# Kernel tuning notes

Hardware: AMD Instinct MI355X
Metric: run time of the kernel (lower is better)

Reference implementation:

```python
import jax, jax.numpy as jnp
import numpy as np

N, L, E, H = 8, 2048, 1024, 1024
EPS = 1e-5


def layernorm(x, g, b):
    m = jnp.mean(x, axis=-1, keepdims=True)
    v = jnp.var(x, axis=-1, keepdims=True)
    return (x - m) * jax.lax.rsqrt(v + EPS) * g + b


def setup_inputs() -> dict:
    key = jax.random.key(0)
    ks = jax.random.split(key, 6)
    s = 0.02
    return {
        "X": jax.random.normal(ks[0], (N, L, E), dtype=jnp.float32),
        "Wq": jax.random.normal(ks[1], (E, H), dtype=jnp.float32) * s,
        "bq": jnp.zeros((H,), jnp.float32),
        "Wk": jax.random.normal(ks[2], (E, H), dtype=jnp.float32) * s,
        "bk": jnp.zeros((H,), jnp.float32),
        "Wv": jax.random.normal(ks[3], (E, H), dtype=jnp.float32) * s,
        "bv": jnp.zeros((H,), jnp.float32),
        "Wf": jax.random.normal(ks[4], (H, H), dtype=jnp.float32) * s,
        "bf": jnp.zeros((H,), jnp.float32),
        "g1": jnp.ones((H,), jnp.float32),
        "b1": jnp.zeros((H,), jnp.float32),
        "g2": jnp.ones((H,), jnp.float32),
        "b2": jnp.zeros((H,), jnp.float32),
    }


def reference(X, Wq, bq, Wk, bk, Wv, bv, Wf, bf, g1, b1, g2, b2):
    scale = 1.0 / jnp.sqrt(jnp.float32(H))
    # both Q and K scaled by 1/sqrt(H) as in source (effective 1/H)
    Q = (X @ Wq + bq) * scale          # (N, L, H)
    K = (X @ Wk + bk) * scale          # (N, L, H)
    V = X @ Wv + bv                    # (N, L, H)
    A = jnp.einsum('nah,nbh->nab', Q, K)   # (N, Lq, Lk)
    A = jax.nn.softmax(A, axis=1)           # softmax over QUERY axis (dim=1), as in source
    # einsum('nll,nlh->nlh') = diagonal of A scaling V elementwise
    diag = jnp.diagonal(A, axis1=1, axis2=2)  # (N, L)
    O = diag[..., None] * V                   # (N, L, H)
    h = layernorm(O + X, g1, b1)
    h = layernorm(h @ Wf + bf + h, g2, b2)
    return h
```

## Files before the change

kernel.cpp:

```cpp
#include <hip/hip_runtime.h>
#include <math.h>

#define NB   8
#define LLEN 2048
#define HDIM 1024
#define LNEPS 1e-5f

#define BM 128
#define BK 64
#define NT_K (HDIM / BK)
#define NT_K8 (HDIM / 128)
#define NTHR 256
#define TB 16384

typedef __attribute__((ext_vector_type(8))) short short8;
typedef __attribute__((ext_vector_type(4))) unsigned short ushort4v;
typedef __attribute__((ext_vector_type(4))) float f32x4;
typedef __attribute__((ext_vector_type(4))) int int4v;
typedef __attribute__((ext_vector_type(8))) int int8v;
typedef __attribute__((ext_vector_type(8))) unsigned char uchar8;

typedef __attribute__((address_space(3))) void lds_void;
typedef const __attribute__((address_space(1))) void glob_void;

__device__ __forceinline__ unsigned short f2bf(float f) {
    union { float f; unsigned u; } v; v.f = f;
    unsigned r = v.u + 0x7FFFu + ((v.u >> 16) & 1u);
    return (unsigned short)(r >> 16);
}
__device__ __forceinline__ float bf2f(unsigned short h) {
    union { unsigned u; float f; } v; v.u = ((unsigned)h) << 16;
    return v.f;
}

__device__ __forceinline__ unsigned char f2fp8(float x) {
    union { float f; unsigned u; } v; v.f = x;
    unsigned s = (v.u >> 24) & 0x80u;
    float a = fabsf(x);
    if (!(a < 448.f)) return (unsigned char)(s | 0x7E);
    int e = (int)((v.u >> 23) & 0xFF) - 127;
    if (e < -6) e = -6;
    float q = rintf(ldexpf(a, 3 - e));
    if (q >= 16.f) { q *= 0.5f; e += 1; }
    int qi = (int)q;
    unsigned byte = (qi < 8) ? (unsigned)qi
                             : (((unsigned)(e + 7) << 3) | (unsigned)(qi - 8));
    return (unsigned char)(s | byte);
}
__device__ __forceinline__ float fp8d(unsigned char b) {
    int e = (b >> 3) & 15, m = b & 7;
    float v = e ? ldexpf((float)(8 + m), e - 10) : ldexpf((float)m, -9);
    return (b & 0x80) ? -v : v;
}

__device__ __forceinline__ unsigned pack4_fp8(float a, float b, float c, float d) {
#if __has_builtin(__builtin_amdgcn_cvt_pk_fp8_f32)
    int r = __builtin_amdgcn_cvt_pk_fp8_f32(a, b, 0, false);
    r = __builtin_amdgcn_cvt_pk_fp8_f32(c, d, r, true);
    return (unsigned)r;
#else
    return (unsigned)f2fp8(a) | ((unsigned)f2fp8(b) << 8)
         | ((unsigned)f2fp8(c) << 16) | ((unsigned)f2fp8(d) << 24);
#endif
}

__device__ __forceinline__ void wg_barrier() {
    asm volatile("" ::: "memory");
    __builtin_amdgcn_s_barrier();
    asm volatile("" ::: "memory");
}

__device__ __forceinline__ void stage128_bf16(
    const unsigned short* __restrict__ src, int R0, int kcol0,
    unsigned short* ldsDst, int w, int l)
{
    const int rsub = l >> 3;
    const int ce = 8 * ((l & 7) ^ rsub);
    #pragma unroll
    for (int s = 0; s < 4; ++s) {
        const int r = s*32 + w*8 + rsub;
        __builtin_amdgcn_global_load_lds(
            (glob_void*)(src + (size_t)(R0 + r) * HDIM + kcol0 + ce),
            (lds_void*)(ldsDst + s*2048 + w*512), 16, 0, 0);
    }
}

__device__ __forceinline__ void stage128_fp8(
    const unsigned char* __restrict__ src, int R0, int kcol0,
    unsigned char* ldsDst, int w, int l)
{
    const int rsub = l >> 3;
    const int cb = ((l & 7) ^ rsub) << 4;
    #pragma unroll
    for (int s = 0; s < 4; ++s) {
        const int r = s*32 + w*8 + rsub;
        __builtin_amdgcn_global_load_lds(
            (glob_void*)(src + (size_t)(R0 + r) * HDIM + kcol0 + cb),
            (lds_void*)(ldsDst + s*4096 + w*1024), 16, 0, 0);
    }
}

__device__ __forceinline__ void pipe128_bf16(
    const unsigned short* __restrict__ srcA,
    const unsigned short* __restrict__ srcB,
    int rowBase, int colBase, int k0, int nt,
    unsigned short* lds, f32x4 (&acc)[4][4])
{
    const int t = threadIdx.x, w = t >> 6, l = t & 63;
    const int wr = w >> 1, wc = w & 1;
    const int lr = l & 15;
    const int sw = (l & 7) << 4;
    const int aRB = (wr*64 + lr) * 128;
    const int bRB = (wc*64 + lr) * 128;
    const int c0 = ((l >> 4) * 16) ^ sw;
    const int c1 = (64 + ((l >> 4) * 16)) ^ sw;

    unsigned short* sA[2] = { lds,          lds + 2*(TB/2) };
    unsigned short* sB[2] = { lds + TB/2,   lds + 3*(TB/2) };

    stage128_bf16(srcA, rowBase, k0,      sA[0], w, l);
    stage128_bf16(srcB, colBase, k0,      sB[0], w, l);
    stage128_bf16(srcA, rowBase, k0 + BK, sA[1], w, l);
    stage128_bf16(srcB, colBase, k0 + BK, sB[1], w, l);
    asm volatile("s_waitcnt vmcnt(8)" ::: "memory");
    wg_barrier();

    for (int kt = 0; kt < nt; ++kt) {
        const char* bufA = (const char*)sA[kt & 1];
        const char* bufB = (const char*)sB[kt & 1];
        #pragma unroll
        for (int kk = 0; kk < 2; ++kk) {
            const int cc = kk ? c1 : c0;
            short8 af[4], bfr[4];
            #pragma unroll
            for (int mi = 0; mi < 4; ++mi)
                af[mi] = *(const short8*)(bufA + aRB + mi*2048 + cc);
            #pragma unroll
            for (int ni = 0; ni < 4; ++ni)
                bfr[ni] = *(const short8*)(bufB + bRB + ni*2048 + cc);
            #pragma unroll
            for (int mi = 0; mi < 4; ++mi)
                #pragma unroll
                for (int ni = 0; ni < 4; ++ni)
                    acc[mi][ni] = __builtin_amdgcn_mfma_f32_16x16x32_bf16(
                        af[mi], bfr[ni], acc[mi][ni], 0, 0, 0);
        }
        if (kt == nt - 1) break;
        wg_barrier();
        if (kt + 2 < nt) {
            stage128_bf16(srcA, rowBase, k0 + (kt+2)*BK, sA[kt&1], w, l);
            stage128_bf16(srcB, colBase, k0 + (kt+2)*BK, sB[kt&1], w, l);
            asm volatile("s_waitcnt vmcnt(8)" ::: "memory");
        } else {
            asm volatile("s_waitcnt vmcnt(0)" ::: "memory");
        }
        wg_barrier();
    }
}

__device__ __forceinline__ void pipe128_fp8(
    const unsigned char* __restrict__ srcA,
    const unsigned char* __restrict__ srcB,
    int rowBase, int colBase,
    unsigned char* lds, f32x4 (&acc)[4][4],
    unsigned sa, unsigned sb)
{
    const int t = threadIdx.x, w = t >> 6, l = t & 63;
    const int wr = w >> 1, wc = w & 1;
    const int lr = l & 15;
    const int sw = (l & 7) << 4;
    const int aRB = (wr*64 + lr) * 128;
    const int bRB = (wc*64 + lr) * 128;
    const int g0 = (l >> 4) * 32;
    const int cc0 = g0 ^ sw;
    const int cc1 = (g0 + 16) ^ sw;

    unsigned char* sA[2] = { lds,        lds + 2*TB };
    unsigned char* sB[2] = { lds + TB,   lds + 3*TB };

    stage128_fp8(srcA, rowBase, 0,   sA[0], w, l);
    stage128_fp8(srcB, colBase, 0,   sB[0], w, l);
    stage128_fp8(srcA, rowBase, 128, sA[1], w, l);
    stage128_fp8(srcB, colBase, 128, sB[1], w, l);
    asm volatile("s_waitcnt vmcnt(8)" ::: "memory");
    wg_barrier();

    for (int kt = 0; kt < NT_K8; ++kt) {
        const char* bufA = (const char*)sA[kt & 1];
        const char* bufB = (const char*)sB[kt & 1];
        int8v b8[4];
        #pragma unroll
        for (int ni = 0; ni < 4; ++ni)
            b8[ni] = __builtin_shufflevector(
                *(const int4v*)(bufB + bRB + ni*2048 + cc0),
                *(const int4v*)(bufB + bRB + ni*2048 + cc1),
                0, 1, 2, 3, 4, 5, 6, 7);
        #pragma unroll
        for (int mi = 0; mi < 4; ++mi) {
            int8v a8 = __builtin_shufflevector(
                *(const int4v*)(bufA + aRB + mi*2048 + cc0),
                *(const int4v*)(bufA + aRB + mi*2048 + cc1),
                0, 1, 2, 3, 4, 5, 6, 7);
            #pragma unroll
            for (int ni = 0; ni < 4; ++ni)
                acc[mi][ni] = __builtin_amdgcn_mfma_scale_f32_16x16x128_f8f6f4(
                    a8, b8[ni], acc[mi][ni], 0, 0, 0, sa, 0, sb);
        }
        if (kt == NT_K8 - 1) break;
        wg_barrier();
        if (kt + 2 < NT_K8) {
            stage128_fp8(srcA, rowBase, (kt+2)*128, sA[kt&1], w, l);
            stage128_fp8(srcB, colBase, (kt+2)*128, sB[kt&1], w, l);
            asm volatile("s_waitcnt vmcnt(8)" ::: "memory");
        } else {
            asm volatile("s_waitcnt vmcnt(0)" ::: "memory");
        }
        wg_barrier();
    }
}

__global__ __launch_bounds__(NTHR) void gemm_proj(
    const unsigned short* __restrict__ A,
    const unsigned short* __restrict__ Bt,
    const float* __restrict__ bias,
    unsigned short* __restrict__ C,
    float alpha, int gx)
{
    __shared__ __align__(16) unsigned short lds[2 * TB];
    const int nwg = gridDim.x, bid = blockIdx.x;
    const int swz = (bid & 7) * (nwg >> 3) + (bid >> 3);
    const int bx = swz % gx, by = swz / gx;
    const int rowBase = by * BM, colBase = bx * BM;

    f32x4 acc[4][4] = {};
    pipe128_bf16(A, Bt, rowBase, colBase, 0, NT_K, lds, acc);

    const int t = threadIdx.x, w = t >> 6, l = t & 63;
    const int wr = w >> 1, wc = w & 1;
    const int lr = l & 15;

    #pragma unroll
    for (int ni = 0; ni < 4; ++ni) {
        const int col = colBase + wc*64 + ni*16 + lr;
        const float bv = bias[col];
        #pragma unroll
        for (int mi = 0; mi < 4; ++mi) {
            const int row0 = rowBase + wr*64 + mi*16 + (l >> 4) * 4;
            #pragma unroll
            for (int j = 0; j < 4; ++j)
                C[(size_t)(row0 + j) * HDIM + col] = f2bf(alpha * (acc[mi][ni][j] + bv));
        }
    }
}

__global__ __launch_bounds__(NTHR) void gemm_wqk_splitk(
    const unsigned short* __restrict__ Wkb,
    const unsigned short* __restrict__ Wqb,
    float* __restrict__ slabs)
{
    __shared__ __align__(16) unsigned short lds[2 * TB];
    const int bid = blockIdx.x;
    const int kz = bid & 3, tile = bid >> 2;
    const int rowBase = (tile >> 3) * BM, colBase = (tile & 7) * BM;

    f32x4 acc[4][4] = {};
    pipe128_bf16(Wkb, Wqb, rowBase, colBase, kz * (HDIM/4), NT_K/4, lds, acc);

    float* out = slabs + (size_t)kz * HDIM * HDIM;
    const int t = threadIdx.x, w = t >> 6, l = t & 63;
    const int wr = w >> 1, wc = w & 1;
    const int lr = l & 15;

    #pragma unroll
    for (int ni = 0; ni < 4; ++ni) {
        const int col = colBase + wc*64 + ni*16 + lr;
        #pragma unroll
        for (int mi = 0; mi < 4; ++mi) {
            const int row0 = rowBase + wr*64 + mi*16 + (l >> 4) * 4;
            #pragma unroll
            for (int j = 0; j < 4; ++j)
                out[(size_t)(row0 + j) * HDIM + col] = acc[mi][ni][j];
        }
    }
}

__global__ __launch_bounds__(256) void wqk_reduce_cast(
    const float* __restrict__ slabs, unsigned char* __restrict__ out8)
{
    const size_t WEl = (size_t)HDIM * HDIM;
    const size_t i = ((size_t)blockIdx.x * 256 + threadIdx.x) * 4;
    float4 a = *reinterpret_cast<const float4*>(slabs + i);
    float4 b = *reinterpret_cast<const float4*>(slabs + WEl + i);
    float4 c = *reinterpret_cast<const float4*>(slabs + 2*WEl + i);
    float4 d = *reinterpret_cast<const float4*>(slabs + 3*WEl + i);
    unsigned wd = pack4_fp8(64.f*(a.x+b.x+c.x+d.x), 64.f*(a.y+b.y+c.y+d.y),
                            64.f*(a.z+b.z+c.z+d.z), 64.f*(a.w+b.w+c.w+d.w));
    *reinterpret_cast<unsigned*>(out8 + i) = wd;
}

__global__ __launch_bounds__(NTHR) void gemm_proj_fp8(
    const unsigned char* __restrict__ A,
    const unsigned char* __restrict__ Bt,
    const float* __restrict__ bias0, const float* __restrict__ bias1,
    unsigned char* __restrict__ C0, unsigned char* __restrict__ C1,
    float al0, float al1, unsigned sb0, unsigned sb1, int gx)
{
    __shared__ __align__(16) unsigned char lds8[4 * TB];
    const int nwg = gridDim.x, bid = blockIdx.x;
    const int swz = (bid & 7) * (nwg >> 3) + (bid >> 3);
    const int bx = swz % gx, by = swz / gx;
    const int rowBase = by * BM, colBase = bx * BM;

    const int mat = colBase >> 10;

    f32x4 acc[4][4] = {};
    pipe128_fp8(A, Bt, rowBase, colBase, lds8, acc,
                0x7F7F7F7Fu, mat ? sb1 : sb0);

    const int t = threadIdx.x, w = t >> 6, l = t & 63;
    const int wr = w >> 1, wc = w & 1;
    const int lr = l & 15;

    unsigned char* Cm  = mat ? C1 : C0;
    const float* bm    = mat ? bias1 : bias0;
    const float am     = mat ? al1 : al0;
    const int lcb = colBase & (HDIM - 1);

    #pragma unroll
    for (int ni = 0; ni < 4; ++ni) {
        const int col = lcb + wc*64 + ni*16 + lr;
        const float bv = bm[col];
        #pragma unroll
        for (int mi = 0; mi < 4; ++mi) {
            const int row0 = rowBase + wr*64 + mi*16 + (l >> 4) * 4;
            const unsigned wd = pack4_fp8(
                am * (acc[mi][ni][0] + bv), am * (acc[mi][ni][1] + bv),
                am * (acc[mi][ni][2] + bv), am * (acc[mi][ni][3] + bv));
            #pragma unroll
            for (int j = 0; j < 4; ++j)
                Cm[(size_t)(row0 + j) * HDIM + col] = (unsigned char)(wd >> (8*j));
        }
    }
}

__global__ __launch_bounds__(NTHR) void qk_colsum_diag_fp8(
    const unsigned char* __restrict__ Xq8,
    const unsigned char* __restrict__ Xb8,
    const float* __restrict__ uvec,
    float* __restrict__ colsum, float* __restrict__ diagv)
{
    __shared__ __align__(16) unsigned char lds8[4 * TB];
    const int bid = blockIdx.x;
    const int n = bid & 7;
    const int rem = bid >> 3;
    const int rowBase = (rem & 15) * BM;
    const int colBase = (rem >> 4) * BM;
    const unsigned char* An = Xq8 + (size_t)n * LLEN * HDIM;
    const unsigned char* Bn = Xb8 + (size_t)n * LLEN * HDIM;

    f32x4 acc[4][4] = {};
    pipe128_fp8(An, Bn, rowBase, colBase, lds8, acc,
                0x75757575u, 0x7F7F7F7Fu);

    const int t = threadIdx.x, w = t >> 6, l = t & 63;
    const int wr = w >> 1, wc = w & 1;
    const int lr = l & 15;

    float ur[4][4];
    #pragma unroll
    for (int mi = 0; mi < 4; ++mi)
        #pragma unroll
        for (int j = 0; j < 4; ++j)
            ur[mi][j] = uvec[(size_t)n * LLEN + rowBase + wr*64 + mi*16 + (l>>4)*4 + j];

    #pragma unroll
    for (int ni = 0; ni < 4; ++ni) {
        float s = 0.f;
        #pragma unroll
        for (int mi = 0; mi < 4; ++mi)
            #pragma unroll
            for (int j = 0; j < 4; ++j)
                s += __expf(acc[mi][ni][j] + ur[mi][j]);
        s += __shfl_xor(s, 16);
        s += __shfl_xor(s, 32);
        if (l < 16)
            atomicAdd(&colsum[(size_t)n * LLEN + colBase + wc*64 + ni*16 + l], s);
    }

    if (rowBase == colBase && wr == wc) {
        #pragma unroll
        for (int mi = 0; mi < 4; ++mi)
            #pragma unroll
            for (int ni = 0; ni < 4; ++ni)
                #pragma unroll
                for (int j = 0; j < 4; ++j) {
                    const int rr = wr*64 + mi*16 + (l >> 4)*4 + j;
                    const int cc = wc*64 + ni*16 + lr;
                    if (rr == cc)
                        diagv[(size_t)n * LLEN + rowBase + rr] = acc[mi][ni][j];
                }
    }
}

__global__ __launch_bounds__(256) void cast_x_dual(
    const float* __restrict__ in, unsigned short* __restrict__ outb,
    unsigned char* __restrict__ out8, int n8)
{
    int i = blockIdx.x * 256 + threadIdx.x;
    if (i >= n8) return;
    const float4* p = reinterpret_cast<const float4*>(in) + (size_t)i * 2;
    float4 a = p[0], b = p[1];
    short8 o;
    o[0] = (short)f2bf(a.x); o[1] = (short)f2bf(a.y);
    o[2] = (short)f2bf(a.z); o[3] = (short)f2bf(a.w);
    o[4] = (short)f2bf(b.x); o[5] = (short)f2bf(b.y);
    o[6] = (short)f2bf(b.z); o[7] = (short)f2bf(b.w);
    unsigned w0 = pack4_fp8(a.x, a.y, a.z, a.w);
    unsigned w1 = pack4_fp8(b.x, b.y, b.z, b.w);
    *(reinterpret_cast<short8*>(outb) + i) = o;
    uint2 pk; pk.x = w0; pk.y = w1;
    *(reinterpret_cast<uint2*>(out8) + i) = pk;
}

__global__ __launch_bounds__(256) void cast_w2(
    const float* __restrict__ W0, const float* __restrict__ W1,
    unsigned short* __restrict__ out0, unsigned short* __restrict__ out1, int n8)
{
    int i = blockIdx.x * 256 + threadIdx.x;
    if (i >= n8) return;
    const float* in = blockIdx.y ? W1 : W0;
    unsigned short* outp = blockIdx.y ? out1 : out0;
    const float4* p = reinterpret_cast<const float4*>(in) + (size_t)i * 2;
    float4 a = p[0], b = p[1];
    short8 o;
    o[0] = (short)f2bf(a.x); o[1] = (short)f2bf(a.y);
    o[2] = (short)f2bf(a.z); o[3] = (short)f2bf(a.w);
    o[4] = (short)f2bf(b.x); o[5] = (short)f2bf(b.y);
    o[6] = (short)f2bf(b.z); o[7] = (short)f2bf(b.w);
    *(reinterpret_cast<short8*>(outp) + i) = o;
}

__global__ __launch_bounds__(256) void transpose_cast_bf16(
    const float* __restrict__ W, unsigned short* __restrict__ Wt)
{
    __shared__ float tile[32][33];
    const int tx = threadIdx.x & 31, ty = threadIdx.x >> 5;
    const int c0 = blockIdx.x * 32, r0 = blockIdx.y * 32;
    #pragma unroll
    for (int r = 0; r < 4; ++r)
        tile[ty + r*8][tx] = W[(size_t)(r0 + ty + r*8) * HDIM + c0 + tx];
    __syncthreads();
    #pragma unroll
    for (int r = 0; r < 4; ++r)
        Wt[(size_t)(c0 + ty + r*8) * HDIM + r0 + tx] = f2bf(tile[tx][ty + r*8]);
}

__global__ __launch_bounds__(256) void transpose_cast_fp8(
    const float* __restrict__ W, unsigned char* __restrict__ Wt, float scale)
{
    __shared__ float tile[32][33];
    const int tx = threadIdx.x & 31, ty = threadIdx.x >> 5;
    const int c0 = blockIdx.x * 32, r0 = blockIdx.y * 32;
    #pragma unroll
    for (int r = 0; r < 4; ++r)
        tile[ty + r*8][tx] = W[(size_t)(r0 + ty + r*8) * HDIM + c0 + tx];
    __syncthreads();
    #pragma unroll
    for (int r = 0; r < 4; ++r)
        Wt[(size_t)(c0 + ty + r*8) * HDIM + r0 + tx] = f2fp8(tile[tx][ty + r*8] * scale);
}

__global__ __launch_bounds__(256) void pvec_kernel(
    const float* __restrict__ Wq, const float* __restrict__ bk,
    float* __restrict__ p)
{
    const int row = blockIdx.x * 4 + (threadIdx.x >> 6);
    const int l = threadIdx.x & 63;
    float s = 0.f;
    #pragma unroll
    for (int c = 0; c < HDIM; c += 64)
        s += Wq[(size_t)row * HDIM + c + l] * bk[c + l];
    #pragma unroll
    for (int off = 32; off > 0; off >>= 1) s += __shfl_down(s, off);
    if (l == 0) p[row] = s;
}

__global__ __launch_bounds__(256) void uvec_kernel(
    const unsigned short* __restrict__ Xb, const float* __restrict__ p,
    float* __restrict__ u, float sc2)
{
    const int row = blockIdx.x * 4 + (threadIdx.x >> 6);
    const int l = threadIdx.x & 63;
    const unsigned short* xr = Xb + (size_t)row * HDIM + l * 16;
    float s = 0.f;
    #pragma unroll
    for (int k = 0; k < 2; ++k) {
        short8 v = *reinterpret_cast<const short8*>(xr + k*8);
        #pragma unroll
        for (int j = 0; j < 8; ++j)
            s += bf2f((unsigned short)v[j]) * p[l*16 + k*8 + j];
    }
    #pragma unroll
    for (int off = 32; off > 0; off >>= 1) s += __shfl_down(s, off);
    if (l == 0) u[row] = s * sc2;
}

__global__ __launch_bounds__(256) void ln1_kernel(
    const unsigned char* __restrict__ V8, const unsigned short* __restrict__ Xbp,
    const float* __restrict__ colsum, const float* __restrict__ diagval,
    const float* __restrict__ uvec,
    const float* __restrict__ g1, const float* __restrict__ b1,
    unsigned short* __restrict__ h1)
{
    const int row = blockIdx.x;
    const size_t base = (size_t)row * HDIM;
    const float dv = __expf(diagval[row] + uvec[row]) / colsum[row];
    const int h0 = threadIdx.x * 4;

    unsigned vv = *reinterpret_cast<const unsigned*>(&V8[base + h0]);
    ushort4v xx = *reinterpret_cast<const ushort4v*>(&Xbp[base + h0]);
    float y[4];
    y[0] = dv * fp8d((unsigned char)(vv      )) + bf2f(xx[0]);
    y[1] = dv * fp8d((unsigned char)(vv >>  8)) + bf2f(xx[1]);
    y[2] = dv * fp8d((unsigned char)(vv >> 16)) + bf2f(xx[2]);
    y[3] = dv * fp8d((unsigned char)(vv >> 24)) + bf2f(xx[3]);

    float s = y[0]+y[1]+y[2]+y[3];
    float s2 = y[0]*y[0]+y[1]*y[1]+y[2]*y[2]+y[3]*y[3];
    #pragma unroll
    for (int off = 32; off > 0; off >>= 1) {
        s  += __shfl_down(s,  off);
        s2 += __shfl_down(s2, off);
    }
    __shared__ float ws1[4], ws2[4];
    const int wid = threadIdx.x >> 6;
    if ((threadIdx.x & 63) == 0) { ws1[wid] = s; ws2[wid] = s2; }
    __syncthreads();
    const float S  = ws1[0]+ws1[1]+ws1[2]+ws1[3];
    const float S2 = ws2[0]+ws2[1]+ws2[2]+ws2[3];
    const float m   = S  * (1.0f / HDIM);
    const float var = S2 * (1.0f / HDIM) - m*m;
    const float inv = rsqrtf(var + LNEPS);

    float4 gg = *reinterpret_cast<const float4*>(&g1[h0]);
    float4 bb = *reinterpret_cast<const float4*>(&b1[h0]);
    ushort4v o;
    o[0] = f2bf((y[0]-m)*inv*gg.x + bb.x);
    o[1] = f2bf((y[1]-m)*inv*gg.y + bb.y);
    o[2] = f2bf((y[2]-m)*inv*gg.z + bb.z);
    o[3] = f2bf((y[3]-m)*inv*gg.w + bb.w);
    *reinterpret_cast<ushort4v*>(&h1[base + h0]) = o;
}

__global__ __launch_bounds__(256) void ln2_kernel(
    const unsigned short* __restrict__ Gb, const unsigned short* __restrict__ h1b,
    const float* __restrict__ g2, const float* __restrict__ b2,
    float* __restrict__ out)
{
    const int row = blockIdx.x;
    const size_t base = (size_t)row * HDIM;
    const int h0 = threadIdx.x * 4;

    ushort4v gv = *reinterpret_cast<const ushort4v*>(&Gb[base + h0]);
    ushort4v hv = *reinterpret_cast<const ushort4v*>(&h1b[base + h0]);
    float y[4];
    y[0] = bf2f(gv[0]) + bf2f(hv[0]); y[1] = bf2f(gv[1]) + bf2f(hv[1]);
    y[2] = bf2f(gv[2]) + bf2f(hv[2]); y[3] = bf2f(gv[3]) + bf2f(hv[3]);

    float s = y[0]+y[1]+y[2]+y[3];
    float s2 = y[0]*y[0]+y[1]*y[1]+y[2]*y[2]+y[3]*y[3];
    #pragma unroll
    for (int off = 32; off > 0; off >>= 1) {
        s  += __shfl_down(s,  off);
        s2 += __shfl_down(s2, off);
    }
    __shared__ float ws1[4], ws2[4];
    const int wid = threadIdx.x >> 6;
    if ((threadIdx.x & 63) == 0) { ws1[wid] = s; ws2[wid] = s2; }
    __syncthreads();
    const float S  = ws1[0]+ws1[1]+ws1[2]+ws1[3];
    const float S2 = ws2[0]+ws2[1]+ws2[2]+ws2[3];
    const float m   = S  * (1.0f / HDIM);
    const float var = S2 * (1.0f / HDIM) - m*m;
    const float inv = rsqrtf(var + LNEPS);

    float4 gg = *reinterpret_cast<const float4*>(&g2[h0]);
    float4 bb = *reinterpret_cast<const float4*>(&b2[h0]);
    float4 o;
    o.x = (y[0]-m)*inv*gg.x + bb.x;
    o.y = (y[1]-m)*inv*gg.y + bb.y;
    o.z = (y[2]-m)*inv*gg.z + bb.z;
    o.w = (y[3]-m)*inv*gg.w + bb.w;
    *reinterpret_cast<float4*>(&out[base + h0]) = o;
}

extern "C" void kernel_launch(void* const* d_in, const int* in_sizes, int n_in,
                              void* d_out, int out_size, void* d_ws, size_t ws_size,
                              hipStream_t stream) {
    (void)in_sizes; (void)n_in; (void)out_size; (void)ws_size;
    const float* X  = (const float*)d_in[0];
    const float* Wq = (const float*)d_in[1];
    const float* bq = (const float*)d_in[2];   (void)bq;
    const float* Wk = (const float*)d_in[3];
    const float* bk = (const float*)d_in[4];
    const float* Wv = (const float*)d_in[5];
    const float* bv = (const float*)d_in[6];
    const float* Wf = (const float*)d_in[7];
    const float* bf = (const float*)d_in[8];
    const float* g1 = (const float*)d_in[9];
    const float* b1 = (const float*)d_in[10];
    const float* g2 = (const float*)d_in[11];
    const float* b2 = (const float*)d_in[12];
    float* out = (float*)d_out;

    const size_t MATE = (size_t)NB * LLEN * HDIM;
    const size_t WE   = (size_t)HDIM * HDIM;

    unsigned short* Xb  = (unsigned short*)d_out;
    unsigned char*  V8  = (unsigned char*)(Xb + MATE);

    unsigned short* h1b   = (unsigned short*)d_ws;
    unsigned short* Gb    = h1b + MATE;
    unsigned short* WfT   = Gb + MATE;
    unsigned short* Wqb   = WfT + WE;
    unsigned short* Wkb   = Wqb + WE;
    unsigned char*  Wqk8T = (unsigned char*)(Wkb + WE);
    unsigned char*  Wv8T  = Wqk8T + WE;
    float* colsum = (float*)(Wv8T + WE);
    float* diagv  = colsum + (size_t)NB * LLEN;
    float* pv     = diagv + (size_t)NB * LLEN;
    float* uv     = pv + HDIM;
    float* zvec   = uv + (size_t)NB * LLEN;
    unsigned char* Xq8 = (unsigned char*)(zvec + HDIM);
    unsigned char* Xb8 = Xq8 + MATE;
    float* wqkSlabs = (float*)(Xb8 + MATE);

    const int M = NB * LLEN;
    const float sc2 = 1.0f / 1024.0f;

    const size_t mset = (3*(size_t)NB*LLEN + 2*HDIM) * sizeof(float);
    hipMemsetAsync(colsum, 0, mset, stream);

    cast_x_dual<<<(int)(MATE/8) / 256, 256, 0, stream>>>(X, Xb, Xb8, (int)(MATE/8));
    {
        dim3 cg((int)(WE/8) / 256, 2);
        cast_w2<<<cg, 256, 0, stream>>>(Wq, Wk, Wqb, Wkb, (int)(WE/8));
    }
    {
        dim3 tgrid(HDIM / 32, HDIM / 32);
        transpose_cast_bf16<<<tgrid, 256, 0, stream>>>(Wf, WfT);
        transpose_cast_fp8<<<tgrid, 256, 0, stream>>>(Wv, Wv8T, 16.0f);
    }

    gemm_wqk_splitk<<<256, NTHR, 0, stream>>>(Wkb, Wqb, wqkSlabs);
    wqk_reduce_cast<<<(int)(WE/4) / 256, 256, 0, stream>>>(wqkSlabs, Wqk8T);

    pvec_kernel<<<HDIM / 4, 256, 0, stream>>>(Wq, bk, pv);
    uvec_kernel<<<M / 4, 256, 0, stream>>>(Xb, pv, uv, sc2);

    {
        const int gx = 2 * HDIM / BM;
        const int nwg = gx * (M / BM);
        gemm_proj_fp8<<<nwg, NTHR, 0, stream>>>(Xb8, Wqk8T, zvec, bv,
                                                Xq8, V8, 1024.0f, 1.0f,
                                                0x6F6F6F6Fu ,
                                                0x7B7B7B7Bu , gx);
    }

    qk_colsum_diag_fp8<<<2048, NTHR, 0, stream>>>(Xq8, Xb8, uv, colsum, diagv);

    ln1_kernel<<<M, 256, 0, stream>>>(V8, Xb, colsum, diagv, uv, g1, b1, h1b);

    {
        const int gx = HDIM / BM;
        const int nwg = gx * (M / BM);
        gemm_proj<<<nwg, NTHR, 0, stream>>>(h1b, WfT, bf, Gb, 1.0f, gx);
    }

    ln2_kernel<<<M, 256, 0, stream>>>(Gb, h1b, g2, b2, out);
}
```

Baseline: 228.5 us.

## Use 256x256 tiles with 512 threads for the feed-forward GEMM

```diff
diff --git a/kernel.cpp b/kernel.cpp
--- a/kernel.cpp
+++ b/kernel.cpp
@@ -12,6 +12,10 @@
 #define NT_K8 (HDIM / 128)
 #define NTHR 256
 #define TB 16384
+
+#define BM2 256
+#define NTHR2 512
+#define SLOT2 (BM2 * BK)
 
 typedef __attribute__((ext_vector_type(8))) short short8;
 typedef __attribute__((ext_vector_type(4))) unsigned short ushort4v;
@@ -219,24 +223,96 @@
     }
 }
 
-__global__ __launch_bounds__(NTHR) void gemm_proj(
+__device__ __forceinline__ void stage256_bf16(
+    const unsigned short* __restrict__ src, int R0, int kcol0,
+    unsigned short* ldsDst, int w, int lane)
+{
+    const int rsub = lane >> 3;
+    const int csw  = 8 * ((lane & 7) ^ rsub);
+    #pragma unroll
+    for (int s = 0; s < 4; ++s) {
+        const int r = (s*8 + w)*8 + rsub;
+        __builtin_amdgcn_global_load_lds(
+            (glob_void*)(src + (size_t)(R0 + r) * HDIM + kcol0 + csw),
+            (lds_void*)(ldsDst + (s*8 + w)*512), 16, 0, 0);
+    }
+}
+
+__device__ __forceinline__ void pipe256_bf16(
+    const unsigned short* __restrict__ srcA,
+    const unsigned short* __restrict__ srcB,
+    int rowBase, int colBase,
+    unsigned short* lds, f32x4 (&acc)[8][4])
+{
+    const int t = threadIdx.x, w = t >> 6, l = t & 63;
+    const int wr = w >> 2, wc = w & 3;
+    const int lr = l & 15;
+    const int sw = (l & 7) << 4;
+    const int aRB = (wr*128 + lr) * 128;
+    const int bRB = (wc*64  + lr) * 128;
+    const int c0 = ((l >> 4) * 16) ^ sw;
+    const int c1 = (64 + ((l >> 4) * 16)) ^ sw;
+
+    unsigned short* sA[2] = { lds,            lds + 2*SLOT2 };
+    unsigned short* sB[2] = { lds + SLOT2,    lds + 3*SLOT2 };
+
+    stage256_bf16(srcA, rowBase, 0,  sA[0], w, l);
+    stage256_bf16(srcB, colBase, 0,  sB[0], w, l);
+    stage256_bf16(srcA, rowBase, BK, sA[1], w, l);
+    stage256_bf16(srcB, colBase, BK, sB[1], w, l);
+    asm volatile("s_waitcnt vmcnt(8)" ::: "memory");
+    wg_barrier();
+
+    for (int kt = 0; kt < NT_K; ++kt) {
+        const char* bufA = (const char*)sA[kt & 1];
+        const char* bufB = (const char*)sB[kt & 1];
+        #pragma unroll
+        for (int kk = 0; kk < 2; ++kk) {
+            const int cc = kk ? c1 : c0;
+            short8 af[8], bfr[4];
+            #pragma unroll
+            for (int mi = 0; mi < 8; ++mi)
+                af[mi] = *(const short8*)(bufA + aRB + mi*2048 + cc);
+            #pragma unroll
+            for (int ni = 0; ni < 4; ++ni)
+                bfr[ni] = *(const short8*)(bufB + bRB + ni*2048 + cc);
+            #pragma unroll
+            for (int mi = 0; mi < 8; ++mi)
+                #pragma unroll
+                for (int ni = 0; ni < 4; ++ni)
+                    acc[mi][ni] = __builtin_amdgcn_mfma_f32_16x16x32_bf16(
+                        af[mi], bfr[ni], acc[mi][ni], 0, 0, 0);
+        }
+        if (kt == NT_K - 1) break;
+        wg_barrier();
+        if (kt + 2 < NT_K) {
+            stage256_bf16(srcA, rowBase, (kt+2)*BK, sA[kt&1], w, l);
+            stage256_bf16(srcB, colBase, (kt+2)*BK, sB[kt&1], w, l);
+            asm volatile("s_waitcnt vmcnt(8)" ::: "memory");
+        } else {
+            asm volatile("s_waitcnt vmcnt(0)" ::: "memory");
+        }
+        wg_barrier();
+    }
+}
+
+__global__ __launch_bounds__(NTHR2, 2) void gemm_ff(
     const unsigned short* __restrict__ A,
     const unsigned short* __restrict__ Bt,
     const float* __restrict__ bias,
-    unsigned short* __restrict__ C,
-    float alpha, int gx)
-{
-    __shared__ __align__(16) unsigned short lds[2 * TB];
+    unsigned short* __restrict__ C, int gx)
+{
+    __shared__ __align__(16) unsigned short lds[4 * SLOT2];
     const int nwg = gridDim.x, bid = blockIdx.x;
     const int swz = (bid & 7) * (nwg >> 3) + (bid >> 3);
     const int bx = swz % gx, by = swz / gx;
-    const int rowBase = by * BM, colBase = bx * BM;
-
-    f32x4 acc[4][4] = {};
-    pipe128_bf16(A, Bt, rowBase, colBase, 0, NT_K, lds, acc);
+    const int rowBase = by * BM2, colBase = bx * BM2;
+
+    f32x4 acc[8][4] = {};
+    pipe256_bf16(A, Bt, rowBase, colBase, lds, acc);
 
     const int t = threadIdx.x, w = t >> 6, l = t & 63;
-    const int wr = w >> 1, wc = w & 1;
+    const int wr = w >> 2, wc = w & 3;
     const int lr = l & 15;
 
     #pragma unroll
@@ -244,11 +320,11 @@
         const int col = colBase + wc*64 + ni*16 + lr;
         const float bv = bias[col];
         #pragma unroll
-        for (int mi = 0; mi < 4; ++mi) {
-            const int row0 = rowBase + wr*64 + mi*16 + (l >> 4) * 4;
+        for (int mi = 0; mi < 8; ++mi) {
+            const int row0 = rowBase + wr*128 + mi*16 + (l >> 4) * 4;
             #pragma unroll
             for (int j = 0; j < 4; ++j)
-                C[(size_t)(row0 + j) * HDIM + col] = f2bf(alpha * (acc[mi][ni][j] + bv));
+                C[(size_t)(row0 + j) * HDIM + col] = f2bf(acc[mi][ni][j] + bv);
         }
     }
 }
@@ -672,9 +748,9 @@
     ln1_kernel<<<M, 256, 0, stream>>>(V8, Xb, colsum, diagv, uv, g1, b1, h1b);
 
     {
-        const int gx = HDIM / BM;
-        const int nwg = gx * (M / BM);
-        gemm_proj<<<nwg, NTHR, 0, stream>>>(h1b, WfT, bf, Gb, 1.0f, gx);
+        const int gx = HDIM / BM2;
+        const int nwg = gx * (M / BM2);
+        gemm_ff<<<nwg, NTHR2, 0, stream>>>(h1b, WfT, bf, Gb, gx);
     }
 
     ln2_kernel<<<M, 256, 0, stream>>>(Gb, h1b, g2, b2, out);
```

New measurement: 209.3 us (median of 2 runs). 1.09x faster.
